# Kernel optimization log

Measured on AMD Instinct MI355X. Metric: run time of the kernel, lower is better.

The kernel has to match this reference:

```python
import jax, jax.numpy as jnp
import numpy as np

NE, S, B, IN, H, L, NL = 16, 16, 256, 61, 1024, 512, 2


def _gru_cell(x, h, wih, whh, bih, bhh):
    # PyTorch GRUCell math, gate order (r, z, n)
    gi = x @ wih.T + bih
    gh = h @ whh.T + bhh
    i_r, i_z, i_n = jnp.split(gi, 3, axis=-1)
    h_r, h_z, h_n = jnp.split(gh, 3, axis=-1)
    r = jax.nn.sigmoid(i_r + h_r)
    z = jax.nn.sigmoid(i_z + h_z)
    n = jnp.tanh(i_n + r * h_n)
    return (1.0 - z) * n + z * h


def setup_inputs():
    key = jax.random.key(0)
    ks = jax.random.split(key, 26)
    def w(i, shape, s=0.05):
        return jax.random.normal(ks[i], shape, jnp.float32) * s
    return {
        "target": jax.random.normal(ks[0], (NE * S, B, IN), jnp.float32),
        "latent": jax.random.normal(ks[1], (B, L), jnp.float32),
        "h0": jnp.zeros((NL, B, H), jnp.float32),
        "h0_dec": jax.random.normal(ks[2], (NE, NL, B, H), jnp.float32),
        "c_wih0": w(3, (3 * H, L)), "c_whh0": w(4, (3 * H, H)),
        "c_bih0": w(5, (3 * H,)), "c_bhh0": w(6, (3 * H,)),
        "c_wih1": w(7, (3 * H, H)), "c_whh1": w(8, (3 * H, H)),
        "c_bih1": w(9, (3 * H,)), "c_bhh1": w(10, (3 * H,)),
        "ce_w": w(11, (L, H)), "ce_b": w(12, (L,)),
        "d_wih0": w(13, (3 * H, IN + L)), "d_whh0": w(14, (3 * H, H)),
        "d_bih0": w(15, (3 * H,)), "d_bhh0": w(16, (3 * H,)),
        "d_wih1": w(17, (3 * H, H)), "d_whh1": w(18, (3 * H, H)),
        "d_bih1": w(19, (3 * H,)), "d_bhh1": w(20, (3 * H,)),
        "o_w": w(21, (IN, H)), "o_b": w(22, (IN,)),
    }


def reference(target, latent, h0, h0_dec,
              c_wih0, c_whh0, c_bih0, c_bhh0,
              c_wih1, c_whh1, c_bih1, c_bhh1,
              ce_w, ce_b,
              d_wih0, d_whh0, d_bih0, d_bhh0,
              d_wih1, d_whh1, d_bih1, d_bhh1,
              o_w, o_b):
    # --- Conductor: NE single-timestep 2-layer GRU steps, same latent input each step ---
    def cond_step(h, _):
        h0n = _gru_cell(latent, h[0], c_wih0, c_whh0, c_bih0, c_bhh0)
        h1n = _gru_cell(h0n, h[1], c_wih1, c_whh1, c_bih1, c_bhh1)
        return jnp.stack([h0n, h1n]), h1n
    _, c_out = jax.lax.scan(cond_step, h0, None, length=NE)  # [NE, B, H]
    emb = jnp.tanh(c_out @ ce_w.T + ce_b)                    # [NE, B, L]

    # --- Decoder (teacher forcing): segments independent -> fold NE into batch ---
    x = target.reshape(NE, S, B, IN).transpose(1, 0, 2, 3)   # [S, NE, B, IN]
    emb_rep = jnp.broadcast_to(emb[None], (S, NE, B, L))
    e = jnp.concatenate([x, emb_rep], axis=-1).reshape(S, NE * B, IN + L)
    hd = h0_dec.transpose(1, 0, 2, 3).reshape(NL, NE * B, H)

    def dec_step(h, xt):
        h0n = _gru_cell(xt, h[0], d_wih0, d_whh0, d_bih0, d_bhh0)
        h1n = _gru_cell(h0n, h[1], d_wih1, d_whh1, d_bih1, d_bhh1)
        return jnp.stack([h0n, h1n]), h1n
    _, y = jax.lax.scan(dec_step, hd, e)                     # [S, NE*B, H]

    probs = jax.nn.softmax(y @ o_w.T + o_b, axis=-1)         # [S, NE*B, IN]
    out = probs.reshape(S, NE, B, IN).transpose(1, 0, 2, 3).reshape(NE * S, B, IN)
    return out
```

## Files before the change

### kernel.cpp

```cpp
#include <hip/hip_runtime.h>
#include <hip/hip_bf16.h>
#include <cstdint>
#include <cstddef>

#define NEc 16
#define SSc 16
#define BBc 256
#define INc 61
#define HHc 1024
#define LLc 512
#define H3c 3072
#define NEBc 4096
#define KXc 64
#define HB  16

typedef __hip_bfloat16 bf16;
typedef __attribute__((ext_vector_type(8))) short bf16x8;
typedef __attribute__((ext_vector_type(4))) float f32x4;
typedef __attribute__((ext_vector_type(4))) short s16x4;

__device__ __forceinline__ void gload16(const void* g, void* l){
    __builtin_amdgcn_global_load_lds((const __attribute__((address_space(1))) unsigned int*)g,
                                     (__attribute__((address_space(3))) unsigned int*)l, 16, 0, 0);
}

__device__ __forceinline__ float sigmoidf_(float x){ return 1.0f/(1.0f+__expf(-x)); }

struct Slice {
    const bf16* A0; int lda0; int K0;
    const bf16* A1; int lda1; int K1;
    const bf16* A2; int lda2;
    const bf16* Wlo;
    const bf16* Whi;
    const float* bp;
    const float* hin;
    float* hout;
    bf16* hbout;
    bf16* out2;
    int mode;
};

#define GRU_KSTEP(APTR, ALDA, ACOL, BPTR, BLDB, BCOL, NIDX)                              \
  {                                                                                      \
    if (!first) __syncthreads();                                                         \
    first = false;                                                                       \
    _Pragma("unroll")                                                                    \
    for (int i=0;i<MR;i++){                                                              \
        const int o = i*4096 + tid*16;                                                   \
        const int u = o ^ (((o>>7)&7)<<4);                                               \
        gload16((APTR) + (size_t)(m0 + (u>>7))*(ALDA) + (ACOL) + ((u&127)>>1), sA + o);  \
    }                                                                                    \
    _Pragma("unroll")                                                                    \
    for (int i=0;i<6;i++){                                                               \
        const int o = i*4096 + tid*16;                                                   \
        const int u = o ^ (((o>>7)&7)<<4);                                               \
        gload16((BPTR) + (size_t)(u>>7)*(BLDB) + (BCOL) + ((u&127)>>1), sB + o);         \
    }                                                                                    \
    __syncthreads();                                                                     \
    _Pragma("unroll")                                                                    \
    for (int ks=0;ks<2;ks++){                                                            \
        bf16x8 av[MR];                                                                   \
        _Pragma("unroll")                                                                \
        for (int mi=0;mi<MR;mi++){                                                       \
            const int r = wm*(BM/2) + mi*16 + lr;                                        \
            const int u = r*128 + ks*64 + lk*16;                                         \
            av[mi] = *(const bf16x8*)(sA + (u ^ ((r&7)<<4)));                            \
        }                                                                                \
        _Pragma("unroll")                                                                \
        for (int hs=0;hs<2;hs++){                                                        \
            _Pragma("unroll")                                                            \
            for (int g3=0;g3<3;g3++){                                                    \
                const int br = ((wc*2+hs)*3 + g3)*16 + lr;                               \
                const int u  = br*128 + ks*64 + lk*16;                                   \
                const bf16x8 bv = *(const bf16x8*)(sB + (u ^ ((br&7)<<4)));              \
                const int gi_ = (g3<2) ? g3 : (NIDX);                                    \
                _Pragma("unroll")                                                        \
                for (int mi=0;mi<MR;mi++)                                                \
                    acc[mi][hs][gi_] = __builtin_amdgcn_mfma_f32_16x16x32_bf16(          \
                        av[mi], bv, acc[mi][hs][gi_], 0,0,0);                            \
            }                                                                            \
        }                                                                                \
    }                                                                                    \
  }

template<int BM>
__device__ void gru_body(const Slice& s, char* smem)
{
    constexpr int MR = BM/32;
    char* sA = smem;
    char* sB = smem + BM*128;

    const int tid  = threadIdx.x;
    const int lane = tid & 63;
    const int wave = tid >> 6;
    const int wm   = wave >> 1;
    const int wc   = wave & 1;
    const int lr   = lane & 15;
    const int lk   = lane >> 4;
    const int hb   = blockIdx.x;
    const int m0   = blockIdx.y * BM;

    const int Klo = s.K0 + s.K1;
    const bf16* WloB = s.Wlo + (size_t)hb*192*Klo;
    const bf16* WhiB = s.Whi + (size_t)hb*192*1024;

    f32x4 acc[MR][2][4];
    #pragma unroll
    for (int mi=0;mi<MR;mi++)
      #pragma unroll
      for (int hs=0;hs<2;hs++)
        #pragma unroll
        for (int g=0;g<4;g++)
          #pragma unroll
          for (int j=0;j<4;j++) acc[mi][hs][g][j] = 0.f;

    bool first = true;

    {
        const bf16* Ap = s.A0; const int Al = s.lda0; const int Kp = s.K0;
        for (int k0 = 0; k0 < Kp; k0 += 64) GRU_KSTEP(Ap, Al, k0, WloB, Klo, k0, 2)
    }
    if (s.K1 > 0){
        const bf16* Ap = s.A1; const int Al = s.lda1; const int Kp = s.K1; const int c0 = s.K0;
        for (int k0 = 0; k0 < Kp; k0 += 64) GRU_KSTEP(Ap, Al, k0, WloB, Klo, c0 + k0, 2)
    }
    {
        const bf16* Ap = s.A2; const int Al = s.lda2;
        for (int k0 = 0; k0 < 1024; k0 += 64) GRU_KSTEP(Ap, Al, k0, WhiB, 1024, k0, 3)
    }

    #pragma unroll
    for (int hs=0;hs<2;hs++){
        const int hsub = wc*2 + hs;
        const int hc   = hb*64 + hsub*16 + lr;
        const float bpr  = s.bp[hb*256 +       hsub*16 + lr];
        const float bpz  = s.bp[hb*256 +  64 + hsub*16 + lr];
        const float bpin = s.bp[hb*256 + 128 + hsub*16 + lr];
        const float bphn = s.bp[hb*256 + 192 + hsub*16 + lr];
        #pragma unroll
        for (int mi=0;mi<MR;mi++)
          #pragma unroll
          for (int j=0;j<4;j++){
            const int rl = wm*(BM/2) + mi*16 + lk*4 + j;
            const int m  = m0 + rl;
            const float r = sigmoidf_(acc[mi][hs][0][j] + bpr);
            const float z = sigmoidf_(acc[mi][hs][1][j] + bpz);
            const float n = tanhf(acc[mi][hs][2][j] + bpin + r*(acc[mi][hs][3][j] + bphn));
            const size_t off = (size_t)m*HHc + hc;
            const float hnew = (1.f - z)*n + z*s.hin[off];
            s.hout[off] = hnew;
            const bf16 hb16 = __float2bfloat16(hnew);
            s.hbout[off] = hb16;
            if (s.out2) s.out2[off] = hb16;
          }
    }
}

__device__ void owsm_body(const Slice& s, char* smem)
{
    if (blockIdx.x != 0) return;
    char* sA = smem; char* sB = smem + 8192;
    const int tid  = threadIdx.x;
    const int lane = tid & 63;
    const int wave = tid >> 6;
    const int wm   = wave >> 1;
    const int wc   = wave & 1;
    const int lr   = lane & 15;
    const int lk   = lane >> 4;
    const int m0   = blockIdx.y * 64;
    const int t    = s.K0;

    f32x4 acc[2][2];
    #pragma unroll
    for (int mi=0;mi<2;mi++)
      #pragma unroll
      for (int ni=0;ni<2;ni++)
        #pragma unroll
        for (int j=0;j<4;j++) acc[mi][ni][j]=0.f;

    for (int k0=0;k0<1024;k0+=64){
        if (k0) __syncthreads();
        #pragma unroll
        for (int i=0;i<2;i++){
            const int o = i*4096 + tid*16;
            const int u = o ^ (((o>>7)&7)<<4);
            gload16(s.A0 + (size_t)(m0 + (u>>7))*1024 + k0 + ((u&127)>>1), sA + o);
        }
        #pragma unroll
        for (int i=0;i<2;i++){
            const int o = i*4096 + tid*16;
            const int u = o ^ (((o>>7)&7)<<4);
            gload16(s.Wlo + (size_t)(u>>7)*1024 + k0 + ((u&127)>>1), sB + o);
        }
        __syncthreads();
        #pragma unroll
        for (int ks=0;ks<2;ks++){
            bf16x8 av[2], bv[2];
            #pragma unroll
            for (int mi=0;mi<2;mi++){
                const int r = wm*32 + mi*16 + lr;
                const int u = r*128 + ks*64 + lk*16;
                av[mi] = *(const bf16x8*)(sA + (u ^ ((r&7)<<4)));
            }
            #pragma unroll
            for (int ni=0;ni<2;ni++){
                const int r = wc*32 + ni*16 + lr;
                const int u = r*128 + ks*64 + lk*16;
                bv[ni] = *(const bf16x8*)(sB + (u ^ ((r&7)<<4)));
            }
            #pragma unroll
            for (int mi=0;mi<2;mi++)
              #pragma unroll
              for (int ni=0;ni<2;ni++)
                acc[mi][ni] = __builtin_amdgcn_mfma_f32_16x16x32_bf16(av[mi], bv[ni], acc[mi][ni], 0,0,0);
        }
    }
    __syncthreads();
    float* lg = (float*)smem;
    #pragma unroll
    for (int mi=0;mi<2;mi++)
      #pragma unroll
      for (int ni=0;ni<2;ni++)
        #pragma unroll
        for (int j=0;j<4;j++){
            const int rl = wm*32 + mi*16 + lk*4 + j;
            const int c  = wc*32 + ni*16 + lr;
            lg[rl*68 + c] = (c < INc) ? (acc[mi][ni][j] + s.bp[c]) : -1e30f;
        }
    __syncthreads();
    const int row = tid >> 2;
    const int q   = tid & 3;
    float mx = -1e30f;
    #pragma unroll
    for (int i=0;i<16;i++) mx = fmaxf(mx, lg[row*68 + q*16+i]);
    mx = fmaxf(mx, __shfl_xor(mx,1));
    mx = fmaxf(mx, __shfl_xor(mx,2));
    float ev[16];
    float sum = 0.f;
    #pragma unroll
    for (int i=0;i<16;i++){ ev[i] = __expf(lg[row*68 + q*16+i] - mx); sum += ev[i]; }
    sum += __shfl_xor(sum,1);
    sum += __shfl_xor(sum,2);
    const float inv = 1.f/sum;
    const int R = m0 + row;
    const int ne = R >> 8, b = R & 255;
    float* op = s.hout + ((size_t)((ne*SSc + t)*BBc + b))*INc;
    #pragma unroll
    for (int i=0;i<16;i++){
        const int c = q*16 + i;
        if (c < INc) op[c] = ev[i]*inv;
    }
}

template<int BM>
__global__ __launch_bounds__(256)
void fused_step(Slice s0, Slice s1, Slice s2)
{
    __shared__ char smem[(BM+192)*128];
    const Slice& s = (blockIdx.z==0) ? s0 : (blockIdx.z==1) ? s1 : s2;
    if (s.mode < 0) return;
    if constexpr (BM>=64){
        if (s.mode == 1){ owsm_body(s, smem); return; }
    }
    gru_body<BM>(s, smem);
}

template<int BM,int BN>
__global__ __launch_bounds__(256)
void gemm_bf(const bf16* __restrict__ A, const bf16* __restrict__ Bm, float* __restrict__ C,
             int K, int ldc)
{
    constexpr int WAVES_M = (BM==128) ? 2 : 1;
    constexpr int WM = BM / WAVES_M;
    constexpr int WN = BN / (4/WAVES_M);
    constexpr int MR = WM / 16;
    constexpr int NR = WN / 16;
    constexpr int ASW = (BM*128)/4096;
    constexpr int BSW = (BN*128)/4096;

    __shared__ char smem[(BM+BN)*128];
    char* sA = smem;
    char* sB = smem + BM*128;

    const int tid  = threadIdx.x;
    const int lane = tid & 63;
    const int wave = tid >> 6;
    const int wm   = (WAVES_M==2) ? (wave>>1) : 0;
    const int wn   = (WAVES_M==2) ? (wave&1)  : wave;
    const int lr   = lane & 15;
    const int lk   = lane >> 4;
    const int m0   = blockIdx.y * BM;
    const int n0   = blockIdx.x * BN;

    f32x4 acc[MR][NR];
    #pragma unroll
    for (int mi=0;mi<MR;mi++)
      #pragma unroll
      for (int ni=0;ni<NR;ni++)
        #pragma unroll
        for (int j=0;j<4;j++) acc[mi][ni][j] = 0.f;

    for (int k0 = 0; k0 < K; k0 += 64){
        if (k0) __syncthreads();
        #pragma unroll
        for (int i=0;i<ASW;i++){
            const int o = i*4096 + tid*16;
            const int u = o ^ (((o>>7)&7)<<4);
            gload16(A + (size_t)(m0 + (u>>7))*K + k0 + ((u&127)>>1), sA + o);
        }
        #pragma unroll
        for (int i=0;i<BSW;i++){
            const int o = i*4096 + tid*16;
            const int u = o ^ (((o>>7)&7)<<4);
            gload16(Bm + (size_t)(n0 + (u>>7))*K + k0 + ((u&127)>>1), sB + o);
        }
        __syncthreads();
        #pragma unroll
        for (int ks=0;ks<2;ks++){
            bf16x8 av[MR], bv[NR];
            #pragma unroll
            for (int mi=0;mi<MR;mi++){
                const int r = wm*WM + mi*16 + lr;
                const int u = r*128 + ks*64 + lk*16;
                av[mi] = *(const bf16x8*)(sA + (u ^ ((r&7)<<4)));
            }
            #pragma unroll
            for (int ni=0;ni<NR;ni++){
                const int r = wn*WN + ni*16 + lr;
                const int u = r*128 + ks*64 + lk*16;
                bv[ni] = *(const bf16x8*)(sB + (u ^ ((r&7)<<4)));
            }
            #pragma unroll
            for (int mi=0;mi<MR;mi++)
              #pragma unroll
              for (int ni=0;ni<NR;ni++)
                acc[mi][ni] = __builtin_amdgcn_mfma_f32_16x16x32_bf16(av[mi], bv[ni], acc[mi][ni], 0,0,0);
        }
    }
    #pragma unroll
    for (int mi=0;mi<MR;mi++)
      #pragma unroll
      for (int ni=0;ni<NR;ni++)
        #pragma unroll
        for (int j=0;j<4;j++){
            const int r = m0 + wm*WM + mi*16 + lk*4 + j;
            const int c = n0 + wn*WN + ni*16 + lr;
            C[(size_t)r*ldc + c] = acc[mi][ni][j];
        }
}

__global__ __launch_bounds__(256) void pack_w2(const float* __restrict__ src, int srcld,
                                               int col0, int Kvalid, int Kchunk,
                                               bf16* __restrict__ dst, int dstld, int dstc0,
                                               int total){
    const int idx = blockIdx.x*256 + threadIdx.x;
    if (idx >= total) return;
    const int k  = idx % Kchunk;
    const int c  = (idx / Kchunk) % 192;
    const int hb = idx / (Kchunk*192);
    const int g  = c >> 4;
    const int hsub = g/3;
    const int gate = g - hsub*3;
    const int row = gate*HHc + hb*64 + hsub*16 + (c & 15);
    const float v = (k < Kvalid) ? src[(size_t)row*srcld + col0 + k] : 0.f;
    dst[((size_t)hb*192 + c)*dstld + dstc0 + k] = __float2bfloat16(v);
}

__global__ __launch_bounds__(256) void pack_bias(const float* __restrict__ bih,
                                                 const float* __restrict__ bhh,
                                                 float* __restrict__ bp){
    const int idx = blockIdx.x*256 + threadIdx.x;
    if (idx >= HB*256) return;
    const int c  = idx & 255;
    const int hb = idx >> 8;
    const int i  = hb*64 + (c&63);
    const int g  = c >> 6;
    float v;
    if      (g==0) v = bih[i] + bhh[i];
    else if (g==1) v = bih[HHc+i] + bhh[HHc+i];
    else if (g==2) v = bih[2*HHc+i];
    else           v = bhh[2*HHc+i];
    bp[idx] = v;
}

__global__ __launch_bounds__(256) void cvt_bf16_k(const float* __restrict__ in, bf16* __restrict__ out, int n4){
    const int i = blockIdx.x*256 + threadIdx.x;
    if (i >= n4) return;
    const f32x4 v = *(const f32x4*)(in + (size_t)i*4);
    union { s16x4 s; bf16 b[4]; } u;
    #pragma unroll
    for (int j=0;j<4;j++) u.b[j] = __float2bfloat16(v[j]);
    *(s16x4*)(out + (size_t)i*4) = u.s;
}

__global__ __launch_bounds__(256) void pad_ow(const float* __restrict__ w, bf16* __restrict__ o){
    const int idx = blockIdx.x*256 + threadIdx.x;
    if (idx >= KXc*HHc) return;
    const int r = idx >> 10;
    o[idx] = __float2bfloat16(r < INc ? w[(size_t)r*HHc + (idx & (HHc-1))] : 0.f);
}

__global__ __launch_bounds__(256) void build_xb(const float* __restrict__ t, bf16* __restrict__ xb){
    const int idx = blockIdx.x*256 + threadIdx.x;
    if (idx >= SSc*NEBc*KXc) return;
    const int c  = idx & 63;
    const int rr = idx >> 6;
    const int s  = rr >> 12;
    const int r  = rr & 4095;
    const int ne = r >> 8;
    const int b  = r & 255;
    const float v = (c < INc) ? t[(((size_t)(ne*SSc + s)*BBc + b)*INc) + c] : 0.f;
    xb[idx] = __float2bfloat16(v);
}

__global__ __launch_bounds__(256) void init_hc(const float* __restrict__ h0,
                                               float* __restrict__ h0c, float* __restrict__ h1c,
                                               bf16* __restrict__ h0cb, bf16* __restrict__ h1cb){
    const int i = blockIdx.x*256 + threadIdx.x;
    if (i >= (BBc*HHc)/4) return;
    const int e = i*4;
    f32x4 a = *(const f32x4*)(h0 + e);
    f32x4 b = *(const f32x4*)(h0 + BBc*HHc + e);
    union { s16x4 v; bf16 q[4]; } ua, ub;
    #pragma unroll
    for (int j=0;j<4;j++){ ua.q[j]=__float2bfloat16(a[j]); ub.q[j]=__float2bfloat16(b[j]); }
    *(f32x4*)(h0c + e) = a; *(f32x4*)(h1c + e) = b;
    *(s16x4*)(h0cb + e) = ua.v; *(s16x4*)(h1cb + e) = ub.v;
}

__global__ __launch_bounds__(256) void init_hd(const float* __restrict__ hd,
                                               float* __restrict__ hd0, float* __restrict__ hd1,
                                               bf16* __restrict__ hd0b, bf16* __restrict__ hd1b){
    const int i = blockIdx.x*256 + threadIdx.x;
    if (i >= (NEBc*HHc)/4) return;
    const int e  = i*4;
    const int hh = e & (HHc-1);
    const int r  = e >> 10;
    const int ne = r >> 8;
    const int b  = r & 255;
    f32x4 a = *(const f32x4*)(hd + (((size_t)ne*2 + 0)*BBc + b)*HHc + hh);
    f32x4 c = *(const f32x4*)(hd + (((size_t)ne*2 + 1)*BBc + b)*HHc + hh);
    union { s16x4 v; bf16 q[4]; } ua, uc;
    #pragma unroll
    for (int j=0;j<4;j++){ ua.q[j]=__float2bfloat16(a[j]); uc.q[j]=__float2bfloat16(c[j]); }
    *(f32x4*)(hd0 + e) = a; *(f32x4*)(hd1 + e) = c;
    *(s16x4*)(hd0b + e) = ua.v; *(s16x4*)(hd1b + e) = uc.v;
}

__global__ __launch_bounds__(256) void bias_tanh4(const float* __restrict__ in,
                                                  const float* __restrict__ b, bf16* __restrict__ out){
    const int i = blockIdx.x*256 + threadIdx.x;
    if (i >= (NEBc*LLc)/4) return;
    const int e = i*4;
    const int c = e & (LLc-1);
    f32x4 v = *(const f32x4*)(in + e);
    f32x4 bb = *(const f32x4*)(b + c);
    union { s16x4 s; bf16 q[4]; } u;
    #pragma unroll
    for (int j=0;j<4;j++) u.q[j] = __float2bfloat16(tanhf(v[j] + bb[j]));
    *(s16x4*)(out + e) = u.s;
}


extern "C" void kernel_launch(void* const* d_in, const int* in_sizes, int n_in,
                              void* d_out, int out_size, void* d_ws, size_t ws_size,
                              hipStream_t stream)
{
    const float* target = (const float*)d_in[0];
    const float* latent = (const float*)d_in[1];
    const float* h0     = (const float*)d_in[2];
    const float* h0_dec = (const float*)d_in[3];
    const float* c_wih0 = (const float*)d_in[4];
    const float* c_whh0 = (const float*)d_in[5];
    const float* c_bih0 = (const float*)d_in[6];
    const float* c_bhh0 = (const float*)d_in[7];
    const float* c_wih1 = (const float*)d_in[8];
    const float* c_whh1 = (const float*)d_in[9];
    const float* c_bih1 = (const float*)d_in[10];
    const float* c_bhh1 = (const float*)d_in[11];
    const float* ce_w   = (const float*)d_in[12];
    const float* ce_b   = (const float*)d_in[13];
    const float* d_wih0 = (const float*)d_in[14];
    const float* d_whh0 = (const float*)d_in[15];
    const float* d_bih0 = (const float*)d_in[16];
    const float* d_bhh0 = (const float*)d_in[17];
    const float* d_wih1 = (const float*)d_in[18];
    const float* d_whh1 = (const float*)d_in[19];
    const float* d_bih1 = (const float*)d_in[20];
    const float* d_bhh1 = (const float*)d_in[21];
    const float* o_w    = (const float*)d_in[22];
    const float* o_b    = (const float*)d_in[23];
    float* out = (float*)d_out;

    float* fp = (float*)d_ws;
    auto fa = [&](size_t n){ float* q = fp; fp += n; return q; };
    float* hd0f[2] = { fa((size_t)NEBc*HHc), fa((size_t)NEBc*HHc) };
    float* hd1f[2] = { fa((size_t)NEBc*HHc), fa((size_t)NEBc*HHc) };
    float* h0cf[2] = { fa((size_t)BBc*HHc),  fa((size_t)BBc*HHc) };
    float* h1cf[2] = { fa((size_t)BBc*HHc),  fa((size_t)BBc*HHc) };
    float* emb   = fa((size_t)NEBc*LLc);
    float* bp_c0 = fa(HB*256);
    float* bp_c1 = fa(HB*256);
    float* bp_d0 = fa(HB*256);
    float* bp_d1 = fa(HB*256);

    bf16* bbp = (bf16*)fp;
    auto ba = [&](size_t n){ bf16* q = bbp; bbp += n; return q; };
    bf16* hd0b[2] = { ba((size_t)NEBc*HHc), ba((size_t)NEBc*HHc) };
    bf16* hd1b[2] = { ba((size_t)NEBc*HHc), ba((size_t)NEBc*HHc) };
    bf16* h0cb[2] = { ba((size_t)BBc*HHc),  ba((size_t)BBc*HHc) };
    bf16* h1cb[2] = { ba((size_t)BBc*HHc),  ba((size_t)BBc*HHc) };
    bf16* xb     = ba((size_t)SSc*NEBc*KXc);
    bf16* coutb  = ba((size_t)NEBc*HHc);
    bf16* embb   = ba((size_t)NEBc*LLc);
    bf16* latb   = ba((size_t)BBc*LLc);
    bf16* Wloc0  = ba((size_t)HB*192*LLc);
    bf16* Whic0  = ba((size_t)HB*192*HHc);
    bf16* Wloc1  = ba((size_t)HB*192*HHc);
    bf16* Whic1  = ba((size_t)HB*192*HHc);
    bf16* Wlod0f = ba((size_t)HB*192*576);
    bf16* Whid0  = ba((size_t)HB*192*HHc);
    bf16* Wlod1  = ba((size_t)HB*192*HHc);
    bf16* Whid1  = ba((size_t)HB*192*HHc);
    bf16* cewb   = ba((size_t)LLc*HHc);
    bf16* owb    = ba((size_t)KXc*HHc);

    auto packw = [&](const float* src, int srcld, int col0, int kv, int kchunk,
                     bf16* dst, int dstld, int dstc0){
        const int tot = HB*192*kchunk;
        hipLaunchKernelGGL(pack_w2, dim3((tot+255)/256), dim3(256),0,stream,
                           src,srcld,col0,kv,kchunk,dst,dstld,dstc0,tot);
    };

    hipLaunchKernelGGL(cvt_bf16_k, dim3((BBc*LLc/4+255)/256), dim3(256),0,stream, latent, latb, BBc*LLc/4);
    hipLaunchKernelGGL(cvt_bf16_k, dim3((LLc*HHc/4+255)/256), dim3(256),0,stream, ce_w, cewb, LLc*HHc/4);
    hipLaunchKernelGGL(pad_ow, dim3((KXc*HHc)/256), dim3(256),0,stream, o_w, owb);
    hipLaunchKernelGGL(build_xb, dim3((SSc*NEBc*KXc)/256), dim3(256),0,stream, target, xb);
    hipLaunchKernelGGL(init_hc, dim3((BBc*HHc/4)/256), dim3(256),0,stream, h0, h0cf[0], h1cf[0], h0cb[0], h1cb[0]);
    hipLaunchKernelGGL(init_hd, dim3((NEBc*HHc/4)/256), dim3(256),0,stream, h0_dec, hd0f[0], hd1f[0], hd0b[0], hd1b[0]);
    packw(c_wih0, LLc,     0,   LLc, LLc,  Wloc0, LLc, 0);
    packw(c_whh0, HHc,     0,   HHc, HHc,  Whic0, HHc, 0);
    packw(c_wih1, HHc,     0,   HHc, HHc,  Wloc1, HHc, 0);
    packw(c_whh1, HHc,     0,   HHc, HHc,  Whic1, HHc, 0);
    packw(d_wih0, INc+LLc, 0,   INc, KXc,  Wlod0f, 576, 0);
    packw(d_wih0, INc+LLc, INc, LLc, LLc,  Wlod0f, 576, KXc);
    packw(d_whh0, HHc,     0,   HHc, HHc,  Whid0, HHc, 0);
    packw(d_wih1, HHc,     0,   HHc, HHc,  Wlod1, HHc, 0);
    packw(d_whh1, HHc,     0,   HHc, HHc,  Whid1, HHc, 0);
    hipLaunchKernelGGL(pack_bias, dim3((HB*256+255)/256), dim3(256),0,stream, c_bih0, c_bhh0, bp_c0);
    hipLaunchKernelGGL(pack_bias, dim3((HB*256+255)/256), dim3(256),0,stream, c_bih1, c_bhh1, bp_c1);
    hipLaunchKernelGGL(pack_bias, dim3((HB*256+255)/256), dim3(256),0,stream, d_bih0, d_bhh0, bp_d0);
    hipLaunchKernelGGL(pack_bias, dim3((HB*256+255)/256), dim3(256),0,stream, d_bih1, d_bhh1, bp_d1);

    auto CL0 = [&](int s){ Slice x{}; x.mode=0;
        x.A0=latb; x.lda0=LLc; x.K0=LLc; x.A1=nullptr; x.lda1=0; x.K1=0;
        x.A2=h0cb[s&1]; x.lda2=HHc; x.Wlo=Wloc0; x.Whi=Whic0; x.bp=bp_c0;
        x.hin=h0cf[s&1]; x.hout=h0cf[(s+1)&1]; x.hbout=h0cb[(s+1)&1]; x.out2=nullptr; return x; };
    auto CL1 = [&](int s){ Slice x{}; x.mode=0;
        x.A0=h0cb[(s+1)&1]; x.lda0=HHc; x.K0=HHc; x.A1=nullptr; x.lda1=0; x.K1=0;
        x.A2=h1cb[s&1]; x.lda2=HHc; x.Wlo=Wloc1; x.Whi=Whic1; x.bp=bp_c1;
        x.hin=h1cf[s&1]; x.hout=h1cf[(s+1)&1]; x.hbout=h1cb[(s+1)&1];
        x.out2=coutb + (size_t)s*BBc*HHc; return x; };
    auto DL0 = [&](int t){ Slice x{}; x.mode=0;
        x.A0=xb + (size_t)t*NEBc*KXc; x.lda0=KXc; x.K0=KXc;
        x.A1=embb; x.lda1=LLc; x.K1=LLc;
        x.A2=hd0b[t&1]; x.lda2=HHc; x.Wlo=Wlod0f; x.Whi=Whid0; x.bp=bp_d0;
        x.hin=hd0f[t&1]; x.hout=hd0f[(t+1)&1]; x.hbout=hd0b[(t+1)&1]; x.out2=nullptr; return x; };
    auto DL1 = [&](int t){ Slice x{}; x.mode=0;
        x.A0=hd0b[(t+1)&1]; x.lda0=HHc; x.K0=HHc; x.A1=nullptr; x.lda1=0; x.K1=0;
        x.A2=hd1b[t&1]; x.lda2=HHc; x.Wlo=Wlod1; x.Whi=Whid1; x.bp=bp_d1;
        x.hin=hd1f[t&1]; x.hout=hd1f[(t+1)&1]; x.hbout=hd1b[(t+1)&1]; x.out2=nullptr; return x; };
    auto OW = [&](int t){ Slice x{}; x.mode=1;
        x.A0=hd1b[(t+1)&1]; x.K0=t; x.Wlo=owb; x.bp=o_b; x.hout=out; return x; };
    Slice NS{}; NS.mode = -1;

    hipLaunchKernelGGL((fused_step<32>), dim3(HB, BBc/32, 1), dim3(256),0,stream, CL0(0), NS, NS);
    for (int s=0;s<NEc;s++){
        if (s < NEc-1)
            hipLaunchKernelGGL((fused_step<32>), dim3(HB, BBc/32, 2), dim3(256),0,stream,
                               CL1(s), CL0(s+1), NS);
        else
            hipLaunchKernelGGL((fused_step<32>), dim3(HB, BBc/32, 1), dim3(256),0,stream,
                               CL1(s), NS, NS);
    }

    hipLaunchKernelGGL((gemm_bf<64,128>), dim3(LLc/128, NEBc/64), dim3(256),0,stream,
                       coutb, cewb, emb, HHc, LLc);
    hipLaunchKernelGGL(bias_tanh4, dim3((NEBc*LLc/4)/256), dim3(256),0,stream, emb, ce_b, embb);

    hipLaunchKernelGGL((fused_step<64>), dim3(HB, NEBc/64, 1), dim3(256),0,stream, DL0(0), NS, NS);
    for (int t=0;t<SSc;t++){
        Slice s1 = (t < SSc-1) ? DL0(t+1) : NS;
        Slice s2 = (t >= 1) ? OW(t-1) : NS;
        const int nz = (t >= 1) ? 3 : 2;
        hipLaunchKernelGGL((fused_step<64>), dim3(HB, NEBc/64, nz), dim3(256),0,stream,
                           DL1(t), s1, s2);
    }
    hipLaunchKernelGGL((fused_step<64>), dim3(1, NEBc/64, 1), dim3(256),0,stream, OW(SSc-1), NS, NS);
}
```

Baseline: 2.860 ms.

## Precompute loop-invariant input projections for conductor and decoder layer 0

```diff
diff --git a/kernel.cpp b/kernel.cpp
--- a/kernel.cpp
+++ b/kernel.cpp
@@ -32,6 +32,7 @@
     const bf16* A2; int lda2;
     const bf16* Wlo;
     const bf16* Whi;
+    const bf16* pre;
     const float* bp;
     const float* hin;
     float* hout;
@@ -143,9 +144,19 @@
           for (int j=0;j<4;j++){
             const int rl = wm*(BM/2) + mi*16 + lk*4 + j;
             const int m  = m0 + rl;
-            const float r = sigmoidf_(acc[mi][hs][0][j] + bpr);
-            const float z = sigmoidf_(acc[mi][hs][1][j] + bpz);
-            const float n = tanhf(acc[mi][hs][2][j] + bpin + r*(acc[mi][hs][3][j] + bphn));
+            float vr  = acc[mi][hs][0][j] + bpr;
+            float vz  = acc[mi][hs][1][j] + bpz;
+            float vin = acc[mi][hs][2][j] + bpin;
+            const float vhn = acc[mi][hs][3][j] + bphn;
+            if (s.pre){
+                const size_t pb = (size_t)m*H3c + hb*192 + hsub*48;
+                vr  += __bfloat162float(s.pre[pb      + lr]);
+                vz  += __bfloat162float(s.pre[pb + 16 + lr]);
+                vin += __bfloat162float(s.pre[pb + 32 + lr]);
+            }
+            const float r = sigmoidf_(vr);
+            const float z = sigmoidf_(vz);
+            const float n = tanhf(vin + r*vhn);
             const size_t off = (size_t)m*HHc + hc;
             const float hnew = (1.f - z)*n + z*s.hin[off];
             s.hout[off] = hnew;
@@ -263,6 +274,80 @@
         if (s.mode == 1){ owsm_body(s, smem); return; }
     }
     gru_body<BM>(s, smem);
+}
+
+__global__ __launch_bounds__(256)
+void gemm_pack(const bf16* __restrict__ A,
+               const bf16* __restrict__ Ep,
+               bf16* __restrict__ C)
+{
+    __shared__ char smem[64*128 + 192*128];
+    char* sA = smem;
+    char* sB = smem + 64*128;
+    const int tid  = threadIdx.x;
+    const int lane = tid & 63;
+    const int wave = tid >> 6;
+    const int wm   = wave >> 1;
+    const int wc   = wave & 1;
+    const int lr   = lane & 15;
+    const int lk   = lane >> 4;
+    const int hb   = blockIdx.x;
+    const int m0   = blockIdx.y * 64;
+    const bf16* Bb = Ep + (size_t)hb*192*512;
+
+    f32x4 acc[2][6];
+    #pragma unroll
+    for (int mi=0;mi<2;mi++)
+      #pragma unroll
+      for (int ni=0;ni<6;ni++)
+        #pragma unroll
+        for (int j=0;j<4;j++) acc[mi][ni][j] = 0.f;
+
+    for (int k0 = 0; k0 < 512; k0 += 64){
+        if (k0) __syncthreads();
+        #pragma unroll
+        for (int i=0;i<2;i++){
+            const int o = i*4096 + tid*16;
+            const int u = o ^ (((o>>7)&7)<<4);
+            gload16(A + (size_t)(m0 + (u>>7))*512 + k0 + ((u&127)>>1), sA + o);
+        }
+        #pragma unroll
+        for (int i=0;i<6;i++){
+            const int o = i*4096 + tid*16;
+            const int u = o ^ (((o>>7)&7)<<4);
+            gload16(Bb + (size_t)(u>>7)*512 + k0 + ((u&127)>>1), sB + o);
+        }
+        __syncthreads();
+        #pragma unroll
+        for (int ks=0;ks<2;ks++){
+            bf16x8 av[2];
+            #pragma unroll
+            for (int mi=0;mi<2;mi++){
+                const int r = wm*32 + mi*16 + lr;
+                const int u = r*128 + ks*64 + lk*16;
+                av[mi] = *(const bf16x8*)(sA + (u ^ ((r&7)<<4)));
+            }
+            #pragma unroll
+            for (int ni=0;ni<6;ni++){
+                const int br = wc*96 + ni*16 + lr;
+                const int u  = br*128 + ks*64 + lk*16;
+                const bf16x8 bv = *(const bf16x8*)(sB + (u ^ ((br&7)<<4)));
+                #pragma unroll
+                for (int mi=0;mi<2;mi++)
+                    acc[mi][ni] = __builtin_amdgcn_mfma_f32_16x16x32_bf16(av[mi], bv, acc[mi][ni], 0,0,0);
+            }
+        }
+    }
+    #pragma unroll
+    for (int mi=0;mi<2;mi++)
+      #pragma unroll
+      for (int ni=0;ni<6;ni++)
+        #pragma unroll
+        for (int j=0;j<4;j++){
+            const int rl = wm*32 + mi*16 + lk*4 + j;
+            const int vc = wc*96 + ni*16 + lr;
+            C[(size_t)(m0+rl)*H3c + hb*192 + vc] = __float2bfloat16(acc[mi][ni][j]);
+        }
 }
 
 template<int BM,int BN>
@@ -514,14 +599,17 @@
     bf16* coutb  = ba((size_t)NEBc*HHc);
     bf16* embb   = ba((size_t)NEBc*LLc);
     bf16* latb   = ba((size_t)BBc*LLc);
-    bf16* Wloc0  = ba((size_t)HB*192*LLc);
+    bf16* giEb   = ba((size_t)NEBc*H3c);
+    bf16* gi0cb  = ba((size_t)BBc*H3c);
     bf16* Whic0  = ba((size_t)HB*192*HHc);
     bf16* Wloc1  = ba((size_t)HB*192*HHc);
     bf16* Whic1  = ba((size_t)HB*192*HHc);
-    bf16* Wlod0f = ba((size_t)HB*192*576);
+    bf16* Wxpk   = ba((size_t)HB*192*KXc);
     bf16* Whid0  = ba((size_t)HB*192*HHc);
     bf16* Wlod1  = ba((size_t)HB*192*HHc);
     bf16* Whid1  = ba((size_t)HB*192*HHc);
+    bf16* Epd    = ba((size_t)HB*192*LLc);
+    bf16* Epc    = ba((size_t)HB*192*LLc);
     bf16* cewb   = ba((size_t)LLc*HHc);
     bf16* owb    = ba((size_t)KXc*HHc);
 
@@ -538,12 +626,12 @@
     hipLaunchKernelGGL(build_xb, dim3((SSc*NEBc*KXc)/256), dim3(256),0,stream, target, xb);
     hipLaunchKernelGGL(init_hc, dim3((BBc*HHc/4)/256), dim3(256),0,stream, h0, h0cf[0], h1cf[0], h0cb[0], h1cb[0]);
     hipLaunchKernelGGL(init_hd, dim3((NEBc*HHc/4)/256), dim3(256),0,stream, h0_dec, hd0f[0], hd1f[0], hd0b[0], hd1b[0]);
-    packw(c_wih0, LLc,     0,   LLc, LLc,  Wloc0, LLc, 0);
     packw(c_whh0, HHc,     0,   HHc, HHc,  Whic0, HHc, 0);
     packw(c_wih1, HHc,     0,   HHc, HHc,  Wloc1, HHc, 0);
     packw(c_whh1, HHc,     0,   HHc, HHc,  Whic1, HHc, 0);
-    packw(d_wih0, INc+LLc, 0,   INc, KXc,  Wlod0f, 576, 0);
-    packw(d_wih0, INc+LLc, INc, LLc, LLc,  Wlod0f, 576, KXc);
+    packw(d_wih0, INc+LLc, 0,   INc, KXc,  Wxpk,  KXc, 0);
+    packw(d_wih0, INc+LLc, INc, LLc, LLc,  Epd,   LLc, 0);
+    packw(c_wih0, LLc,     0,   LLc, LLc,  Epc,   LLc, 0);
     packw(d_whh0, HHc,     0,   HHc, HHc,  Whid0, HHc, 0);
     packw(d_wih1, HHc,     0,   HHc, HHc,  Wlod1, HHc, 0);
     packw(d_whh1, HHc,     0,   HHc, HHc,  Whid1, HHc, 0);
@@ -552,23 +640,25 @@
     hipLaunchKernelGGL(pack_bias, dim3((HB*256+255)/256), dim3(256),0,stream, d_bih0, d_bhh0, bp_d0);
     hipLaunchKernelGGL(pack_bias, dim3((HB*256+255)/256), dim3(256),0,stream, d_bih1, d_bhh1, bp_d1);
 
+    hipLaunchKernelGGL(gemm_pack, dim3(HB, BBc/64), dim3(256),0,stream, latb, Epc, gi0cb);
+
     auto CL0 = [&](int s){ Slice x{}; x.mode=0;
-        x.A0=latb; x.lda0=LLc; x.K0=LLc; x.A1=nullptr; x.lda1=0; x.K1=0;
-        x.A2=h0cb[s&1]; x.lda2=HHc; x.Wlo=Wloc0; x.Whi=Whic0; x.bp=bp_c0;
+        x.A0=nullptr; x.lda0=0; x.K0=0; x.A1=nullptr; x.lda1=0; x.K1=0;
+        x.A2=h0cb[s&1]; x.lda2=HHc; x.Wlo=Whic0; x.Whi=Whic0; x.pre=gi0cb; x.bp=bp_c0;
         x.hin=h0cf[s&1]; x.hout=h0cf[(s+1)&1]; x.hbout=h0cb[(s+1)&1]; x.out2=nullptr; return x; };
     auto CL1 = [&](int s){ Slice x{}; x.mode=0;
         x.A0=h0cb[(s+1)&1]; x.lda0=HHc; x.K0=HHc; x.A1=nullptr; x.lda1=0; x.K1=0;
-        x.A2=h1cb[s&1]; x.lda2=HHc; x.Wlo=Wloc1; x.Whi=Whic1; x.bp=bp_c1;
+        x.A2=h1cb[s&1]; x.lda2=HHc; x.Wlo=Wloc1; x.Whi=Whic1; x.pre=nullptr; x.bp=bp_c1;
         x.hin=h1cf[s&1]; x.hout=h1cf[(s+1)&1]; x.hbout=h1cb[(s+1)&1];
         x.out2=coutb + (size_t)s*BBc*HHc; return x; };
     auto DL0 = [&](int t){ Slice x{}; x.mode=0;
         x.A0=xb + (size_t)t*NEBc*KXc; x.lda0=KXc; x.K0=KXc;
-        x.A1=embb; x.lda1=LLc; x.K1=LLc;
-        x.A2=hd0b[t&1]; x.lda2=HHc; x.Wlo=Wlod0f; x.Whi=Whid0; x.bp=bp_d0;
+        x.A1=nullptr; x.lda1=0; x.K1=0;
+        x.A2=hd0b[t&1]; x.lda2=HHc; x.Wlo=Wxpk; x.Whi=Whid0; x.pre=giEb; x.bp=bp_d0;
         x.hin=hd0f[t&1]; x.hout=hd0f[(t+1)&1]; x.hbout=hd0b[(t+1)&1]; x.out2=nullptr; return x; };
     auto DL1 = [&](int t){ Slice x{}; x.mode=0;
         x.A0=hd0b[(t+1)&1]; x.lda0=HHc; x.K0=HHc; x.A1=nullptr; x.lda1=0; x.K1=0;
-        x.A2=hd1b[t&1]; x.lda2=HHc; x.Wlo=Wlod1; x.Whi=Whid1; x.bp=bp_d1;
+        x.A2=hd1b[t&1]; x.lda2=HHc; x.Wlo=Wlod1; x.Whi=Whid1; x.pre=nullptr; x.bp=bp_d1;
         x.hin=hd1f[t&1]; x.hout=hd1f[(t+1)&1]; x.hbout=hd1b[(t+1)&1]; x.out2=nullptr; return x; };
     auto OW = [&](int t){ Slice x{}; x.mode=1;
         x.A0=hd1b[(t+1)&1]; x.K0=t; x.Wlo=owb; x.bp=o_b; x.hout=out; return x; };
@@ -587,6 +677,7 @@
     hipLaunchKernelGGL((gemm_bf<64,128>), dim3(LLc/128, NEBc/64), dim3(256),0,stream,
                        coutb, cewb, emb, HHc, LLc);
     hipLaunchKernelGGL(bias_tanh4, dim3((NEBc*LLc/4)/256), dim3(256),0,stream, emb, ce_b, embb);
+    hipLaunchKernelGGL(gemm_pack, dim3(HB, NEBc/64), dim3(256),0,stream, embb, Epd, giEb);
 
     hipLaunchKernelGGL((fused_step<64>), dim3(HB, NEBc/64, 1), dim3(256),0,stream, DL0(0), NS, NS);
     for (int t=0;t<SSc;t++){
```

Result: no change. 2.911 ms (+1.8%).
